# Optimization experiments

Hardware: AMD Instinct MI355X
Metric: run time of the kernel (lower is better)

The kernel has to match this reference:

```python
import jax, jax.numpy as jnp
import numpy as np

DK = 64


def setup_inputs() -> dict:
    key = jax.random.key(0)
    k1, k2, k3, k4 = jax.random.split(key, 4)
    B, T, C = 16, 2048, 384
    # Glorot-like scale for projections
    s = (6.0 / (C + DK)) ** 0.5
    return {
        "x": jax.random.normal(k1, (B, T, C), dtype=jnp.float32),
        "WQ": jax.random.uniform(k2, (C, DK), minval=-s, maxval=s, dtype=jnp.float32),
        "WK": jax.random.uniform(k3, (C, DK), minval=-s, maxval=s, dtype=jnp.float32),
        "WV": jax.random.uniform(k4, (C, DK), minval=-s, maxval=s, dtype=jnp.float32),
    }


def reference(x, WQ, WK, WV):
    # x: [B, T, C]; single-head causal self-attention (training=False -> no dropout)
    T = x.shape[1]
    q = jnp.einsum("btc,cd->btd", x, WQ)  # [B, T, dk]
    k = jnp.einsum("btc,cd->btd", x, WK)
    v = jnp.einsum("btc,cd->btd", x, WV)
    scale = 1.0 / jnp.sqrt(jnp.asarray(DK, dtype=x.dtype))
    wei = jnp.einsum("bqd,bkd->bqk", q, k) * scale  # [B, T, T]
    # additive causal mask: -1e9 above the diagonal (matches TF band_part construction)
    causal = jnp.tril(jnp.ones((T, T), dtype=x.dtype))
    wei = wei + (1.0 - causal) * jnp.asarray(-1e9, dtype=x.dtype)
    wei = jax.nn.softmax(wei, axis=-1)
    out = jnp.einsum("bqk,bkd->bqd", wei, v)  # [B, T, dk]
    return out
```

## Files before the change

kernel.cpp:

```cpp
#include <hip/hip_runtime.h>
#include <hip/hip_bf16.h>
#include <math.h>

#define B_  16
#define T_  2048
#define C_  384
#define DK_ 64

typedef short bf16x8 __attribute__((ext_vector_type(8)));
typedef float f32x4  __attribute__((ext_vector_type(4)));
typedef unsigned short u16;
typedef unsigned int   u32;

__device__ __forceinline__ u16 f2bf(float f) {
  u32 u = __builtin_bit_cast(u32, f);
  u32 r = u + 0x7FFFu + ((u >> 16) & 1u);
  return (u16)(r >> 16);
}

__device__ __forceinline__ void gld_lds16(const void* g, void* l) {
  __builtin_amdgcn_global_load_lds(
      (const __attribute__((address_space(1))) void*)g,
      (__attribute__((address_space(3))) void*)l, 16, 0, 0);
}

__device__ __forceinline__ f32x4 mfma16(bf16x8 a, bf16x8 b, f32x4 c) {
  return __builtin_amdgcn_mfma_f32_16x16x32_bf16(a, b, c, 0, 0, 0);
}

__global__ __launch_bounds__(256) void prep_w_k(
    const float* __restrict__ WQ, const float* __restrict__ WK,
    const float* __restrict__ WV, u16* __restrict__ wt) {
  int gi = blockIdx.x * 256 + threadIdx.x;
  if (gi >= 192 * 48) return;
  int n = gi / 48;
  int g = gi - n * 48;
  int k0 = g * 8;
  const float* W = (n < 64) ? WQ : ((n < 128) ? WK : WV);
  int   nn = n & 63;
  float sc = (n < 64) ? 0.18033688011112042f : 1.0f;
  bf16x8 o;
#pragma unroll
  for (int j = 0; j < 8; ++j)
    o[j] = (short)f2bf(W[(size_t)(k0 + j) * DK_ + nn] * sc);
  *(bf16x8*)(wt + (size_t)gi * 8) = o;
}

__global__ __launch_bounds__(256) void proj_k(
    const float* __restrict__ x, const u16* __restrict__ wt,
    u16* __restrict__ qo, u16* __restrict__ ko, u16* __restrict__ vo) {
  int tid = threadIdx.x;
  int w = tid >> 6, lane = tid & 63, l15 = lane & 15, lg = lane >> 4;
  int row0 = (blockIdx.x * 4 + w) * 16;

  f32x4 acc[12];
#pragma unroll
  for (int i = 0; i < 12; ++i) acc[i] = (f32x4){0.f, 0.f, 0.f, 0.f};

  const float* xp0 = x + (size_t)(row0 + l15) * C_ + lg * 8;
#pragma unroll
  for (int ks = 0; ks < 12; ++ks) {
    float4 alo = *(const float4*)(xp0 + ks * 32);
    float4 ahi = *(const float4*)(xp0 + ks * 32 + 4);
    bf16x8 af;
    af[0] = (short)f2bf(alo.x); af[1] = (short)f2bf(alo.y);
    af[2] = (short)f2bf(alo.z); af[3] = (short)f2bf(alo.w);
    af[4] = (short)f2bf(ahi.x); af[5] = (short)f2bf(ahi.y);
    af[6] = (short)f2bf(ahi.z); af[7] = (short)f2bf(ahi.w);
#pragma unroll
    for (int nt = 0; nt < 12; ++nt) {
      bf16x8 bfg = *(const bf16x8*)(wt + (size_t)(nt * 16 + l15) * C_ + ks * 32 + lg * 8);
      acc[nt] = mfma16(af, bfg, acc[nt]);
    }
  }
#pragma unroll
  for (int nt = 0; nt < 12; ++nt) {
    int col = nt * 16 + l15;
    int c = col & 63;
#pragma unroll
    for (int r = 0; r < 4; ++r) {
      int row = row0 + lg * 4 + r;
      u16 val = f2bf(acc[nt][r]);
      if (col < 64)       qo[(size_t)row * DK_ + c] = val;
      else if (col < 128) ko[(size_t)row * DK_ + c] = val;
      else                vo[(size_t)row * DK_ + c] = val;
    }
  }
}

__global__ __launch_bounds__(256) void flash_k(
    const u16* __restrict__ q, const u16* __restrict__ k,
    const u16* __restrict__ v, float* __restrict__ out) {
  __shared__ u16 ldsK[64 * 64];
  __shared__ u16 ldsVT[64 * 64];
  __shared__ u16 ldsP[4 * 16 * 64];

  int tid = threadIdx.x;
  int w = tid >> 6, lane = tid & 63, l15 = lane & 15, lg = lane >> 4;
  int bb = blockIdx.x & 15;
  int qt = 31 - (blockIdx.x >> 4);
  int qrow0 = bb * T_ + qt * 64;

  const u16* qp = q + (size_t)(qrow0 + w * 16 + l15) * DK_ + lg * 8;
  bf16x8 qf0 = *(const bf16x8*)qp;
  bf16x8 qf1 = *(const bf16x8*)(qp + 32);

  f32x4 o[4];
#pragma unroll
  for (int i = 0; i < 4; ++i) o[i] = (f32x4){0.f, 0.f, 0.f, 0.f};
  float m[4], lsum[4];
#pragma unroll
  for (int r = 0; r < 4; ++r) { m[r] = -INFINITY; lsum[r] = 0.f; }

  char* pbuf = (char*)ldsP + w * 2048;

  for (int t = 0; t <= qt; ++t) {
    __syncthreads();
    int kvb = bb * T_ + t * 64;

#pragma unroll
    for (int it = 0; it < 2; ++it) {
      int i = it * 256 + tid;
      int r = i >> 3, s = i & 7;
      gld_lds16(k + (size_t)(kvb + r) * DK_ + ((s ^ (r & 7)) * 8),
                (char*)ldsK + (it * 256 + w * 64) * 16);
    }
    {
      int kv = (tid >> 3) * 2;
      int d0 = (tid & 7) * 8;
      bf16x8 r0 = *(const bf16x8*)(v + (size_t)(kvb + kv) * DK_ + d0);
      bf16x8 r1 = *(const bf16x8*)(v + (size_t)(kvb + kv + 1) * DK_ + d0);
#pragma unroll
      for (int j = 0; j < 8; ++j) {
        int d = d0 + j;
        u32 val = (u32)(u16)r0[j] | ((u32)(u16)r1[j] << 16);
        int off = d * 128 + ((kv * 2) ^ ((((d & 7) ^ ((d >> 3) & 7))) << 4));
        *(u32*)((char*)ldsVT + off) = val;
      }
    }
    __syncthreads();

    f32x4 sa[4];
#pragma unroll
    for (int nt = 0; nt < 4; ++nt) {
      int n = nt * 16 + l15;
      bf16x8 kb0 = *(const bf16x8*)((char*)ldsK + (n * 8 + ((lg) ^ (n & 7))) * 16);
      bf16x8 kb1 = *(const bf16x8*)((char*)ldsK + (n * 8 + ((4 + lg) ^ (n & 7))) * 16);
      sa[nt] = (f32x4){0.f, 0.f, 0.f, 0.f};
      sa[nt] = mfma16(qf0, kb0, sa[nt]);
      sa[nt] = mfma16(qf1, kb1, sa[nt]);
    }

    if (t == qt) {
      int rowt = w * 16 + lg * 4;
#pragma unroll
      for (int nt = 0; nt < 4; ++nt) {
        int colt = nt * 16 + l15;
#pragma unroll
        for (int r = 0; r < 4; ++r)
          if (colt > rowt + r) sa[nt][r] = -INFINITY;
      }
    }

#pragma unroll
    for (int r = 0; r < 4; ++r) {
      float mx = fmaxf(fmaxf(sa[0][r], sa[1][r]), fmaxf(sa[2][r], sa[3][r]));
      mx = fmaxf(mx, __shfl_xor(mx, 1));
      mx = fmaxf(mx, __shfl_xor(mx, 2));
      mx = fmaxf(mx, __shfl_xor(mx, 4));
      mx = fmaxf(mx, __shfl_xor(mx, 8));
      float mn = fmaxf(m[r], mx);
      float al = exp2f(m[r] - mn);
      m[r] = mn;
      float rs = 0.f;
#pragma unroll
      for (int nt = 0; nt < 4; ++nt) {
        float p = exp2f(sa[nt][r] - mn);
        sa[nt][r] = p;
        rs += p;
      }
      rs += __shfl_xor(rs, 1); rs += __shfl_xor(rs, 2);
      rs += __shfl_xor(rs, 4); rs += __shfl_xor(rs, 8);
      lsum[r] = lsum[r] * al + rs;
      o[0][r] *= al; o[1][r] *= al; o[2][r] *= al; o[3][r] *= al;
    }

#pragma unroll
    for (int nt = 0; nt < 4; ++nt) {
#pragma unroll
      for (int r = 0; r < 4; ++r) {
        float pv = sa[nt][r];
        float po = __shfl_xor(pv, 1);
        u32 pk = (lane & 1) ? ((u32)f2bf(po) | ((u32)f2bf(pv) << 16))
                            : ((u32)f2bf(pv) | ((u32)f2bf(po) << 16));
        if (!(lane & 1)) {
          int row = lg * 4 + r;
          int off = row * 128 + ((((nt * 16 + l15) & ~1) * 2) ^ ((row & 7) << 4));
          *(u32*)(pbuf + off) = pk;
        }
      }
    }

    bf16x8 pf0, pf1;
    {
      int row = l15;
      int sw = (row & 7) << 4;
      pf0 = *(const bf16x8*)(pbuf + row * 128 + (((lg * 8) * 2) ^ sw));
      pf1 = *(const bf16x8*)(pbuf + row * 128 + (((32 + lg * 8) * 2) ^ sw));
    }
#pragma unroll
    for (int dt = 0; dt < 4; ++dt) {
      int d = dt * 16 + l15;
      int swv = ((d & 7) ^ ((d >> 3) & 7)) << 4;
      bf16x8 vf0 = *(const bf16x8*)((char*)ldsVT + d * 128 + (((lg * 8) * 2) ^ swv));
      bf16x8 vf1 = *(const bf16x8*)((char*)ldsVT + d * 128 + (((32 + lg * 8) * 2) ^ swv));
      o[dt] = mfma16(pf0, vf0, o[dt]);
      o[dt] = mfma16(pf1, vf1, o[dt]);
    }
  }

  float rl[4];
#pragma unroll
  for (int r = 0; r < 4; ++r) rl[r] = 1.f / lsum[r];
#pragma unroll
  for (int dt = 0; dt < 4; ++dt)
#pragma unroll
    for (int r = 0; r < 4; ++r)
      out[(size_t)(qrow0 + w * 16 + lg * 4 + r) * DK_ + dt * 16 + l15] =
          o[dt][r] * rl[r];
}

extern "C" void kernel_launch(void* const* d_in, const int* in_sizes, int n_in,
                              void* d_out, int out_size, void* d_ws, size_t ws_size,
                              hipStream_t stream) {
  const float* x  = (const float*)d_in[0];
  const float* WQ = (const float*)d_in[1];
  const float* WK = (const float*)d_in[2];
  const float* WV = (const float*)d_in[3];
  float* out = (float*)d_out;

  char* ws = (char*)d_ws;
  u16* qb = (u16*)(ws);
  u16* kb = (u16*)(ws + ((size_t)4 << 20));
  u16* vb = (u16*)(ws + ((size_t)8 << 20));
  u16* wt = (u16*)(ws + ((size_t)12 << 20));

  prep_w_k<<<36, 256, 0, stream>>>(WQ, WK, WV, wt);
  proj_k<<<512, 256, 0, stream>>>(x, wt, qb, kb, vb);
  flash_k<<<512, 256, 0, stream>>>(qb, kb, vb, out);
}
```

Measured before the change: 224.9 us.

## Split KV range across blocks in flash attention and add merge kernel

The flash kernel now splits each query tile's causal KV loop across up to four blocks, striding tiles by the split count. Each block writes its unnormalized partial output plus running max and sum to workspace, and a new merge kernel combines them with log-sum-exp rescaling. The projection kernel is also split in half along output columns so it launches twice as many blocks. The split targets load imbalance and low occupancy from the triangular causal workload, at the cost of extra global traffic for partials and an additional kernel launch.

```diff
diff --git a/kernel.cpp b/kernel.cpp
--- a/kernel.cpp
+++ b/kernel.cpp
@@ -51,14 +51,17 @@
     u16* __restrict__ qo, u16* __restrict__ ko, u16* __restrict__ vo) {
   int tid = threadIdx.x;
   int w = tid >> 6, lane = tid & 63, l15 = lane & 15, lg = lane >> 4;
-  int row0 = (blockIdx.x * 4 + w) * 16;
-
-  f32x4 acc[12];
-#pragma unroll
-  for (int i = 0; i < 12; ++i) acc[i] = (f32x4){0.f, 0.f, 0.f, 0.f};
+  int half = blockIdx.x & 1;
+  int row0 = ((blockIdx.x >> 1) * 4 + w) * 16;
+  int cbase = half * 96;
+
+  f32x4 acc[6];
+#pragma unroll
+  for (int i = 0; i < 6; ++i) acc[i] = (f32x4){0.f, 0.f, 0.f, 0.f};
 
   const float* xp0 = x + (size_t)(row0 + l15) * C_ + lg * 8;
-#pragma unroll
+  const u16*   wb  = wt + (size_t)(cbase + l15) * C_ + lg * 8;
+#pragma unroll 2
   for (int ks = 0; ks < 12; ++ks) {
     float4 alo = *(const float4*)(xp0 + ks * 32);
     float4 ahi = *(const float4*)(xp0 + ks * 32 + 4);
@@ -68,37 +71,40 @@
     af[4] = (short)f2bf(ahi.x); af[5] = (short)f2bf(ahi.y);
     af[6] = (short)f2bf(ahi.z); af[7] = (short)f2bf(ahi.w);
 #pragma unroll
-    for (int nt = 0; nt < 12; ++nt) {
-      bf16x8 bfg = *(const bf16x8*)(wt + (size_t)(nt * 16 + l15) * C_ + ks * 32 + lg * 8);
+    for (int nt = 0; nt < 6; ++nt) {
+      bf16x8 bfg = *(const bf16x8*)(wb + (size_t)nt * 16 * C_ + ks * 32);
       acc[nt] = mfma16(af, bfg, acc[nt]);
     }
   }
 #pragma unroll
-  for (int nt = 0; nt < 12; ++nt) {
-    int col = nt * 16 + l15;
-    int c = col & 63;
+  for (int nt = 0; nt < 6; ++nt) {
+    int col = cbase + nt * 16 + l15;
 #pragma unroll
     for (int r = 0; r < 4; ++r) {
       int row = row0 + lg * 4 + r;
       u16 val = f2bf(acc[nt][r]);
-      if (col < 64)       qo[(size_t)row * DK_ + c] = val;
-      else if (col < 128) ko[(size_t)row * DK_ + c] = val;
-      else                vo[(size_t)row * DK_ + c] = val;
+      if (col < 64)       qo[(size_t)row * DK_ + col] = val;
+      else if (col < 128) ko[(size_t)row * DK_ + (col - 64)] = val;
+      else                vo[(size_t)row * DK_ + (col - 128)] = val;
     }
   }
 }
 
 __global__ __launch_bounds__(256) void flash_k(
     const u16* __restrict__ q, const u16* __restrict__ k,
-    const u16* __restrict__ v, float* __restrict__ out) {
+    const u16* __restrict__ v, float* __restrict__ pO,
+    float* __restrict__ pML, int lgS) {
   __shared__ u16 ldsK[64 * 64];
   __shared__ u16 ldsVT[64 * 64];
   __shared__ u16 ldsP[4 * 16 * 64];
 
+  int Sv = 1 << lgS;
+  int s   = blockIdx.x & (Sv - 1);
+  int idx = blockIdx.x >> lgS;
   int tid = threadIdx.x;
   int w = tid >> 6, lane = tid & 63, l15 = lane & 15, lg = lane >> 4;
-  int bb = blockIdx.x & 15;
-  int qt = 31 - (blockIdx.x >> 4);
+  int bb = idx & 15;
+  int qt = 31 - (idx >> 4);
   int qrow0 = bb * T_ + qt * 64;
 
   const u16* qp = q + (size_t)(qrow0 + w * 16 + l15) * DK_ + lg * 8;
@@ -114,15 +120,15 @@
 
   char* pbuf = (char*)ldsP + w * 2048;
 
-  for (int t = 0; t <= qt; ++t) {
+  for (int t = s; t <= qt; t += Sv) {
     __syncthreads();
     int kvb = bb * T_ + t * 64;
 
 #pragma unroll
     for (int it = 0; it < 2; ++it) {
       int i = it * 256 + tid;
-      int r = i >> 3, s = i & 7;
-      gld_lds16(k + (size_t)(kvb + r) * DK_ + ((s ^ (r & 7)) * 8),
+      int r = i >> 3, ss = i & 7;
+      gld_lds16(k + (size_t)(kvb + r) * DK_ + ((ss ^ (r & 7)) * 8),
                 (char*)ldsK + (it * 256 + w * 64) * 16);
     }
     {
@@ -219,15 +225,50 @@
     }
   }
 
-  float rl[4];
-#pragma unroll
-  for (int r = 0; r < 4; ++r) rl[r] = 1.f / lsum[r];
+  float* po = pO + (((size_t)idx << lgS) + s) * 4096;
 #pragma unroll
   for (int dt = 0; dt < 4; ++dt)
 #pragma unroll
     for (int r = 0; r < 4; ++r)
-      out[(size_t)(qrow0 + w * 16 + lg * 4 + r) * DK_ + dt * 16 + l15] =
-          o[dt][r] * rl[r];
+      po[(w * 16 + lg * 4 + r) * 64 + dt * 16 + l15] = o[dt][r];
+  if (l15 == 0) {
+    float* pm = pML + (((size_t)idx << lgS) + s) * 128;
+#pragma unroll
+    for (int r = 0; r < 4; ++r) {
+      pm[w * 16 + lg * 4 + r]      = m[r];
+      pm[64 + w * 16 + lg * 4 + r] = lsum[r];
+    }
+  }
+}
+
+__global__ __launch_bounds__(256) void merge_k(
+    const float* __restrict__ pO, const float* __restrict__ pML,
+    float* __restrict__ out, int lgS) {
+  int Sv = 1 << lgS;
+  int idx = blockIdx.x;
+  int bb = idx & 15, qt = 31 - (idx >> 4);
+  int row = threadIdx.x >> 2, cg = threadIdx.x & 3;
+
+  const float* pm = pML + ((size_t)idx << lgS) * 128;
+  float mstar = -INFINITY;
+  for (int s = 0; s < Sv; ++s) mstar = fmaxf(mstar, pm[s * 128 + row]);
+
+  float lstar = 0.f;
+  float acc[16];
+#pragma unroll
+  for (int c = 0; c < 16; ++c) acc[c] = 0.f;
+  const float* po = pO + ((size_t)idx << lgS) * 4096 + row * 64 + cg * 16;
+  for (int s = 0; s < Sv; ++s) {
+    float wsc = exp2f(pm[s * 128 + row] - mstar);
+    lstar += wsc * pm[s * 128 + 64 + row];
+    const float* ps = po + (size_t)s * 4096;
+#pragma unroll
+    for (int c = 0; c < 16; ++c) acc[c] += wsc * ps[c];
+  }
+  float inv = 1.f / lstar;
+  size_t orow = (size_t)(bb * T_ + qt * 64 + row) * DK_ + cg * 16;
+#pragma unroll
+  for (int c = 0; c < 16; ++c) out[orow + c] = acc[c] * inv;
 }
 
 extern "C" void kernel_launch(void* const* d_in, const int* in_sizes, int n_in,
@@ -245,7 +286,16 @@
   u16* vb = (u16*)(ws + ((size_t)8 << 20));
   u16* wt = (u16*)(ws + ((size_t)12 << 20));
 
+  size_t pbase = (size_t)16 << 20;
+  int lgS = 2;
+  if (ws_size < pbase + (size_t)512 * 4 * (4096 + 128) * 4) lgS = 1;
+  if (ws_size < pbase + (size_t)512 * 2 * (4096 + 128) * 4) lgS = 0;
+  size_t S = (size_t)1 << lgS;
+  float* pO  = (float*)(ws + pbase);
+  float* pML = (float*)(ws + pbase + (size_t)512 * S * 4096 * 4);
+
   prep_w_k<<<36, 256, 0, stream>>>(WQ, WK, WV, wt);
-  proj_k<<<512, 256, 0, stream>>>(x, wt, qb, kb, vb);
-  flash_k<<<512, 256, 0, stream>>>(qb, kb, vb, out);
-}
+  proj_k<<<1024, 256, 0, stream>>>(x, wt, qb, kb, vb);
+  flash_k<<<512 << lgS, 256, 0, stream>>>(qb, kb, vb, pO, pML, lgS);
+  merge_k<<<512, 256, 0, stream>>>(pO, pML, out, lgS);
+}
```

New measurement: 189.1 us. -15.9%, faster.
